# Performance work log

Measured on AMD Instinct MI355X. Metric: run time of the kernel, lower is better.

## Reference

```python
import jax, jax.numpy as jnp
import numpy as np

EPS = 1e-5  # torch LayerNorm default

def ln(x, g, b):
    mu = jnp.mean(x, axis=-1, keepdims=True)
    var = jnp.mean((x - mu) ** 2, axis=-1, keepdims=True)
    return (x - mu) * jax.lax.rsqrt(var + EPS) * g + b

B, S, E, A = 131072, 199, 3, 32
D_IN = S + 1  # state_dim + 1 (time feature)

def setup_inputs() -> dict:
    key = jax.random.key(0)
    ks = iter(jax.random.split(key, 32))
    def w(shape, fan_in):
        lim = 1.0 / np.sqrt(fan_in)
        return jax.random.uniform(next(ks), shape, jnp.float32, -lim, lim)
    inp = {
        "state": jax.random.normal(next(ks), (B, S), jnp.float32),
        "time_delta": jax.random.uniform(next(ks), (B,), jnp.float32),
        # trunk: Linear(200,256)+LN, Linear(256,256)+LN, Linear(256,128)+LN
        "W1": w((D_IN, 256), D_IN), "b1": w((256,), D_IN),
        "g1": jnp.ones((256,), jnp.float32), "be1": jnp.zeros((256,), jnp.float32),
        "W2": w((256, 256), 256), "b2": w((256,), 256),
        "g2": jnp.ones((256,), jnp.float32), "be2": jnp.zeros((256,), jnp.float32),
        "W3": w((256, 128), 256), "b3": w((128,), 256),
        "g3": jnp.ones((128,), jnp.float32), "be3": jnp.zeros((128,), jnp.float32),
        # value stream
        "Wv1": w((128, 64), 128), "bv1": w((64,), 128),
        "gv": jnp.ones((64,), jnp.float32), "bev": jnp.zeros((64,), jnp.float32),
        "Wv2": w((64, 1), 64), "bv2": w((1,), 64),
        # E stacked advantage streams (all heads share action dim A)
        "Wa1": w((E, 128, 64), 128), "ba1": w((E, 64), 128),
        "ga": jnp.ones((E, 64), jnp.float32), "bea": jnp.zeros((E, 64), jnp.float32),
        "Wa2": w((E, 64, A), 64), "ba2": w((E, A), 64),
        "event_type": jax.random.randint(next(ks), (B,), 0, E),
    }
    return inp

def reference(state, time_delta,
              W1, b1, g1, be1, W2, b2, g2, be2, W3, b3, g3, be3,
              Wv1, bv1, gv, bev, Wv2, bv2,
              Wa1, ba1, ga, bea, Wa2, ba2, event_type):
    td = time_delta[:, None]                       # [B,1]
    x = jnp.concatenate([state, td], axis=1)       # [B,200]
    h = jax.nn.relu(ln(x @ W1 + b1, g1, be1))      # [B,256]
    h = jax.nn.relu(ln(h @ W2 + b2, g2, be2))      # [B,256]
    f = jax.nn.relu(ln(h @ W3 + b3, g3, be3))      # [B,128]
    v = jax.nn.relu(ln(f @ Wv1 + bv1, gv, bev)) @ Wv2 + bv2  # [B,1]
    # compute all E advantage heads, then per-sample select by event_type
    h1 = jnp.einsum('bd,edh->ebh', f, Wa1) + ba1[:, None, :]           # [E,B,64]
    h1 = jax.nn.relu(ln(h1, ga[:, None, :], bea[:, None, :]))
    adv_all = jnp.einsum('ebh,eha->eba', h1, Wa2) + ba2[:, None, :]    # [E,B,A]
    adv = jnp.take_along_axis(adv_all, event_type[None, :, None], axis=0)[0]  # [B,A]
    return v + (adv - adv.mean(axis=1, keepdims=True))
```

## Files before the change

### kernel.cpp

```cpp
#include <hip/hip_runtime.h>
#include <hip/hip_bf16.h>
#include <stdint.h>

#define DEV __device__ __forceinline__

typedef __attribute__((ext_vector_type(8))) short short8;
typedef __attribute__((ext_vector_type(4))) float floatx4;

constexpr int TM  = 64;
constexpr int NB  = 131072;
constexpr int AST = 264;

constexpr int OFF_W1 = 0;
constexpr int OFF_W2 = 57344;
constexpr int OFF_W3 = 122880;
constexpr int OFF_WH = 155648;
constexpr int OFF_WA2= 188416;
constexpr int NWQ    = 194560;

constexpr int C_B1=0, C_G1=256, C_BE1=512, C_B2=768, C_G2=1024, C_BE2=1280,
  C_B3=1536, C_G3=1664, C_BE3=1792, C_BV1=1920, C_GV=1984, C_BEV=2048,
  C_WV2=2112, C_BV2=2176, C_BA1=2180, C_GA=2372, C_BEA=2564, C_BA2=2756;
constexpr int NCONST=2852;

struct Ptrs {
  const float *state,*td,*W1,*b1,*g1,*be1,*W2,*b2,*g2,*be2,*W3,*b3,*g3,*be3,
    *Wv1,*bv1,*gv,*bev,*Wv2,*bv2,*Wa1,*ba1,*ga,*bea,*Wa2,*ba2;
  const int *et;
};

DEV unsigned short f2bf(float x){
  uint32_t u = __float_as_uint(x);
  u += 0x7fffu + ((u>>16)&1u);
  return (unsigned short)(u>>16);
}
DEV uint32_t f2bf_pk(float a, float b){
  float2 f2; f2.x=a; f2.y=b;
  __hip_bfloat162 h = __float22bfloat162_rn(f2);
  union { __hip_bfloat162 h; uint32_t u; } cv; cv.h = h;
  return cv.u;
}

__global__ void prep_kernel(Ptrs p, unsigned short* __restrict__ wq, float* __restrict__ cq){
  int idx = blockIdx.x*256 + threadIdx.x;
  if (idx < NWQ) {
    float v = 0.f;
    if (idx < OFF_W2) {
      int e = idx, w = e/14336, r = e%14336;
      int kc = r>>11, ct=(r>>9)&3, l=(r>>3)&63, j=r&7;
      int n = w*64 + ct*16 + (l&15);
      int k = kc*32 + (l>>4)*8 + j;
      if (k < 200) v = p.W1[k*256 + n];
      else if (k == 200) v = p.b1[n];
    } else if (idx < OFF_W3) {
      int e = idx-OFF_W2, w=e>>14, r=e&16383;
      int kc=r>>11, ct=(r>>9)&3, l=(r>>3)&63, j=r&7;
      int n = w*64 + ct*16 + (l&15);
      int k = kc*32 + (l>>4)*8 + j;
      v = p.W2[k*256 + n];
    } else if (idx < OFF_WH) {
      int e = idx-OFF_W3, w=e>>13, r=e&8191;
      int kc=r>>10, ct=(r>>9)&1, l=(r>>3)&63, j=r&7;
      int n = w*32 + ct*16 + (l&15);
      int k = kc*32 + (l>>4)*8 + j;
      v = p.W3[k*128 + n];
    } else if (idx < OFF_WA2) {
      int e = idx-OFF_WH, h=e>>13, r=e&8191;
      int kc=r>>11, ct=(r>>9)&3, l=(r>>3)&63, j=r&7;
      int n = ct*16 + (l&15);
      int k = kc*32 + (l>>4)*8 + j;
      v = (h<3) ? p.Wa1[h*8192 + k*64 + n] : p.Wv1[k*64 + n];
    } else {
      int e = idx-OFF_WA2, h=e>>11, r=e&2047;
      int kc=r>>10, ct=(r>>9)&1, l=(r>>3)&63, j=r&7;
      int n = ct*16 + (l&15);
      int k = kc*32 + (l>>4)*8 + j;
      v = p.Wa2[h*2048 + k*32 + n];
    }
    wq[idx] = f2bf(v);
  } else if (idx < NWQ + NCONST) {
    int ci = idx - NWQ;
    float v;
    if      (ci < 256)  v = p.b1[ci];
    else if (ci < 512)  v = p.g1[ci-256];
    else if (ci < 768)  v = p.be1[ci-512];
    else if (ci < 1024) v = p.b2[ci-768];
    else if (ci < 1280) v = p.g2[ci-1024];
    else if (ci < 1536) v = p.be2[ci-1280];
    else if (ci < 1664) v = p.b3[ci-1536];
    else if (ci < 1792) v = p.g3[ci-1664];
    else if (ci < 1920) v = p.be3[ci-1792];
    else if (ci < 1984) v = p.bv1[ci-1920];
    else if (ci < 2048) v = p.gv[ci-1984];
    else if (ci < 2112) v = p.bev[ci-2048];
    else if (ci < 2176) v = p.Wv2[ci-2112];
    else if (ci < 2180) v = (ci==2176) ? p.bv2[0] : 0.f;
    else if (ci < 2372) v = p.ba1[ci-2180];
    else if (ci < 2564) v = p.ga[ci-2372];
    else if (ci < 2756) v = p.bea[ci-2564];
    else                v = p.ba2[ci-2756];
    cq[ci] = v;
  }
}

template<int N>
DEV void loadB(short8 (&B)[N], const unsigned short* __restrict__ src, int lane){
  #pragma unroll
  for (int i=0;i<N;i++) B[i] = *(const short8*)(src + i*512 + lane*8);
}

template<int RT>
DEV void zeroAccT(floatx4 (&acc)[RT][4]){
  const floatx4 z = {0.f,0.f,0.f,0.f};
  #pragma unroll
  for (int rt=0;rt<RT;rt++)
    #pragma unroll
    for (int ct=0;ct<4;ct++) acc[rt][ct]=z;
}

template<int KC,int RT>
DEV void runGemmT(floatx4 (&acc)[RT][4], const short8 (&Bw)[KC*RT],
                  const unsigned short* aBase, int aOff){
  #pragma unroll
  for (int kc=0;kc<KC;kc++){
    short8 a[4];
    #pragma unroll
    for (int ct=0;ct<4;ct++)
      a[ct] = *(const short8*)(aBase + ct*16*AST + aOff + kc*32);
    #pragma unroll
    for (int rt=0;rt<RT;rt++)
      #pragma unroll
      for (int ct=0;ct<4;ct++)
        acc[rt][ct] = __builtin_amdgcn_mfma_f32_16x16x32_bf16(Bw[kc*RT+rt], a[ct], acc[rt][ct], 0,0,0);
  }
}

template<int RT,bool BIAS>
DEV void statsT(floatx4 (&acc)[RT][4], const float* __restrict__ cq, int bo,
                float* sbuf, float* ssbuf, int q, int ln){
  if constexpr (BIAS){
    #pragma unroll
    for (int rt=0;rt<RT;rt++){
      floatx4 b4 = *(const floatx4*)(cq + bo + rt*16 + q*4);
      #pragma unroll
      for (int ct=0;ct<4;ct++) acc[rt][ct] += b4;
    }
  }
  #pragma unroll
  for (int ct=0;ct<4;ct++){
    float s=0.f, ss=0.f;
    #pragma unroll
    for (int rt=0;rt<RT;rt++)
      #pragma unroll
      for (int r=0;r<4;r++){ float v=acc[rt][ct][r]; s+=v; ss+=v*v; }
    s += __shfl_xor(s,16); ss += __shfl_xor(ss,16);
    s += __shfl_xor(s,32); ss += __shfl_xor(ss,32);
    if (q==0){
      atomicAdd(&sbuf[ct*16+ln], s);
      atomicAdd(&ssbuf[ct*16+ln], ss);
    }
  }
}

template<int RT>
DEV void lnWriteT(const floatx4 (&acc)[RT][4], const float* __restrict__ cq, int go, int beo,
                  const float* sbuf, const float* ssbuf, float invN,
                  unsigned short* act_, int colBase, int q, int ln){
  float mu[4], rs[4];
  #pragma unroll
  for (int ct=0;ct<4;ct++){
    float sv = sbuf[ct*16+ln], ssv = ssbuf[ct*16+ln];
    mu[ct] = sv*invN;
    rs[ct] = rsqrtf(ssv*invN - mu[ct]*mu[ct] + 1e-5f);
  }
  #pragma unroll
  for (int rt=0;rt<RT;rt++){
    floatx4 g4  = *(const floatx4*)(cq + go  + rt*16 + q*4);
    floatx4 be4 = *(const floatx4*)(cq + beo + rt*16 + q*4);
    #pragma unroll
    for (int ct=0;ct<4;ct++){
      float y[4];
      #pragma unroll
      for (int r=0;r<4;r++)
        y[r] = fmaxf((acc[rt][ct][r]-mu[ct])*rs[ct]*g4[r]+be4[r], 0.f);
      uint2 pk; pk.x = f2bf_pk(y[0],y[1]); pk.y = f2bf_pk(y[2],y[3]);
      *(uint2*)(act_ + (ct*16+ln)*AST + colBase + rt*16 + q*4) = pk;
    }
  }
}

__global__ __launch_bounds__(256,4) void dqn_main(
    const float* __restrict__ state, const float* __restrict__ td,
    const int* __restrict__ et, const unsigned short* __restrict__ wq,
    const float* __restrict__ cq, float* __restrict__ out)
{
  __shared__ __align__(16) unsigned short act[TM*AST];
  __shared__ float sstat[2][2][64];
  __shared__ float vbuf[64];
  __shared__ int   etl[64];

  const int tid=threadIdx.x, w=tid>>6, lane=tid&63, q=lane>>4, ln=lane&15;
  const int rowBlk = blockIdx.x*TM;

  {
    ((float*)sstat)[tid] = 0.f;
    const float* sbase = state + (size_t)rowBlk*199;
    #pragma unroll
    for (int it=0; it<7; ++it){
      int t = tid + it*256;
      int r = t/28, c = t - r*28;
      unsigned short* dst = act + r*AST + c*8;
      if (c < 25){
        const float* src = sbase + r*199 + c*8;
        float v0=src[0], v1=src[1], v2=src[2], v3=src[3];
        float v4=src[4], v5=src[5], v6=src[6];
        int o7 = (c==24)? 198 : c*8+7;
        float s7 = sbase[r*199 + o7];
        float v7 = (c==24)? td[rowBlk+r] : s7;
        uint4 pk;
        pk.x=f2bf_pk(v0,v1); pk.y=f2bf_pk(v2,v3);
        pk.z=f2bf_pk(v4,v5); pk.w=f2bf_pk(v6,v7);
        *(uint4*)dst = pk;
      } else {
        uint4 pk{0u,0u,0u,0u};
        if (c==25) pk.x = 0x3F80u;
        *(uint4*)dst = pk;
      }
    }
    if (tid < 64) etl[tid] = et[rowBlk+tid];
  }
  __syncthreads();

  const unsigned short* aBase = act + ln*AST + q*8;
  floatx4 acc[4][4];

  {
    short8 Bw[28];
    loadB<28>(Bw, wq + OFF_W1 + w*14336, lane);
    zeroAccT<4>(acc);
    runGemmT<7,4>(acc, Bw, aBase, 0);
  }
  statsT<4,false>(acc, cq, 0, sstat[0][0], sstat[0][1], q, ln);
  __syncthreads();
  lnWriteT<4>(acc, cq, C_G1+w*64, C_BE1+w*64, sstat[0][0], sstat[0][1], 1.f/256.f, act, w*64, q, ln);
  __syncthreads();

  {
    short8 Bw[32];
    loadB<32>(Bw, wq + OFF_W2 + w*16384, lane);
    zeroAccT<4>(acc);
    runGemmT<8,4>(acc, Bw, aBase, 0);
  }
  statsT<4,true>(acc, cq, C_B2+w*64, sstat[1][0], sstat[1][1], q, ln);
  __syncthreads();
  if (tid < 128) ((float*)sstat[0])[tid] = 0.f;
  lnWriteT<4>(acc, cq, C_G2+w*64, C_BE2+w*64, sstat[1][0], sstat[1][1], 1.f/256.f, act, w*64, q, ln);
  __syncthreads();

  floatx4 acc3[2][4];
  {
    short8 Bw[16];
    loadB<16>(Bw, wq + OFF_W3 + w*8192, lane);
    zeroAccT<2>(acc3);
    runGemmT<8,2>(acc3, Bw, aBase, 0);
  }
  statsT<2,true>(acc3, cq, C_B3+w*32, sstat[0][0], sstat[0][1], q, ln);
  __syncthreads();
  lnWriteT<2>(acc3, cq, C_G3+w*32, C_BE3+w*32, sstat[0][0], sstat[0][1], 1.f/128.f, act, w*32, q, ln);
  __syncthreads();

  {
    short8 Bh[16];
    loadB<16>(Bh, wq + OFF_WH + w*8192, lane);
    zeroAccT<4>(acc);
    runGemmT<4,4>(acc, Bh, aBase, 0);
  }
  {
    const int bo = (w<3)? C_BA1+w*64 : C_BV1;
    const int go = (w<3)? C_GA +w*64 : C_GV;
    const int beo= (w<3)? C_BEA+w*64 : C_BEV;
    #pragma unroll
    for (int rt=0;rt<4;rt++){
      floatx4 b4 = *(const floatx4*)(cq + bo + rt*16 + q*4);
      #pragma unroll
      for (int ct=0;ct<4;ct++) acc[rt][ct] += b4;
    }
    float mu[4], rs[4];
    #pragma unroll
    for (int ct=0;ct<4;ct++){
      float s=0.f, ss=0.f;
      #pragma unroll
      for (int rt=0;rt<4;rt++)
        #pragma unroll
        for (int r=0;r<4;r++){ float v=acc[rt][ct][r]; s+=v; ss+=v*v; }
      s += __shfl_xor(s,16); ss += __shfl_xor(ss,16);
      s += __shfl_xor(s,32); ss += __shfl_xor(ss,32);
      mu[ct]=s*(1.f/64.f);
      rs[ct]=rsqrtf(ss*(1.f/64.f)-mu[ct]*mu[ct]+1e-5f);
    }
    #pragma unroll
    for (int rt=0;rt<4;rt++){
      floatx4 g4  = *(const floatx4*)(cq + go  + rt*16 + q*4);
      floatx4 be4 = *(const floatx4*)(cq + beo + rt*16 + q*4);
      #pragma unroll
      for (int ct=0;ct<4;ct++)
        #pragma unroll
        for (int r=0;r<4;r++)
          acc[rt][ct][r] = fmaxf((acc[rt][ct][r]-mu[ct])*rs[ct]*g4[r]+be4[r], 0.f);
    }
    if (w==3){
      float bv2v = cq[C_BV2];
      floatx4 wv4[4];
      #pragma unroll
      for (int rt=0;rt<4;rt++) wv4[rt] = *(const floatx4*)(cq + C_WV2 + rt*16 + q*4);
      #pragma unroll
      for (int ct=0;ct<4;ct++){
        float dot=0.f;
        #pragma unroll
        for (int rt=0;rt<4;rt++)
          #pragma unroll
          for (int r=0;r<4;r++) dot += acc[rt][ct][r]*wv4[rt][r];
        dot += __shfl_xor(dot,16);
        dot += __shfl_xor(dot,32);
        if (q==0) vbuf[ct*16+ln] = dot + bv2v;
      }
    }
  }
  __syncthreads();

  if (w<3){
    #pragma unroll
    for (int rt=0;rt<4;rt++)
      #pragma unroll
      for (int ct=0;ct<4;ct++){
        uint2 pk;
        pk.x = f2bf_pk(acc[rt][ct][0], acc[rt][ct][1]);
        pk.y = f2bf_pk(acc[rt][ct][2], acc[rt][ct][3]);
        *(uint2*)(act + (ct*16+ln)*AST + 64*w + rt*16 + q*4) = pk;
      }
    short8 B2[4];
    loadB<4>(B2, wq + OFF_WA2 + w*2048, lane);
    floatx4 acc2[2][4];
    zeroAccT<2>(acc2);
    runGemmT<2,2>(acc2, B2, aBase, 64*w);
    #pragma unroll
    for (int rt=0;rt<2;rt++){
      floatx4 b4 = *(const floatx4*)(cq + C_BA2 + w*32 + rt*16 + q*4);
      #pragma unroll
      for (int ct=0;ct<4;ct++) acc2[rt][ct] += b4;
    }
    #pragma unroll
    for (int ct=0;ct<4;ct++){
      float sm=0.f;
      #pragma unroll
      for (int rt=0;rt<2;rt++)
        #pragma unroll
        for (int r=0;r<4;r++) sm += acc2[rt][ct][r];
      sm += __shfl_xor(sm,16);
      sm += __shfl_xor(sm,32);
      int b = ct*16+ln;
      if (etl[b]==w){
        float vm = vbuf[b] - sm*(1.f/32.f);
        #pragma unroll
        for (int rt=0;rt<2;rt++){
          floatx4 o = acc2[rt][ct];
          o[0]+=vm; o[1]+=vm; o[2]+=vm; o[3]+=vm;
          *(floatx4*)(out + (size_t)(rowBlk+b)*32 + rt*16 + q*4) = o;
        }
      }
    }
  }
}

extern "C" void kernel_launch(void* const* d_in, const int* in_sizes, int n_in,
                              void* d_out, int out_size, void* d_ws, size_t ws_size,
                              hipStream_t stream)
{
  Ptrs p;
  p.state=(const float*)d_in[0];  p.td =(const float*)d_in[1];
  p.W1 =(const float*)d_in[2];  p.b1 =(const float*)d_in[3];  p.g1 =(const float*)d_in[4];  p.be1=(const float*)d_in[5];
  p.W2 =(const float*)d_in[6];  p.b2 =(const float*)d_in[7];  p.g2 =(const float*)d_in[8];  p.be2=(const float*)d_in[9];
  p.W3 =(const float*)d_in[10]; p.b3 =(const float*)d_in[11]; p.g3 =(const float*)d_in[12]; p.be3=(const float*)d_in[13];
  p.Wv1=(const float*)d_in[14]; p.bv1=(const float*)d_in[15]; p.gv =(const float*)d_in[16]; p.bev=(const float*)d_in[17];
  p.Wv2=(const float*)d_in[18]; p.bv2=(const float*)d_in[19];
  p.Wa1=(const float*)d_in[20]; p.ba1=(const float*)d_in[21]; p.ga =(const float*)d_in[22]; p.bea=(const float*)d_in[23];
  p.Wa2=(const float*)d_in[24]; p.ba2=(const float*)d_in[25];
  p.et =(const int*)d_in[26];

  unsigned short* wq = (unsigned short*)d_ws;
  float* cq = (float*)((char*)d_ws + (size_t)NWQ*2);

  const int prepN = NWQ + NCONST;
  hipLaunchKernelGGL(prep_kernel, dim3((prepN+255)/256), dim3(256), 0, stream, p, wq, cq);
  hipLaunchKernelGGL(dqn_main, dim3(NB/TM), dim3(256), 0, stream,
                     p.state, p.td, p.et, (const unsigned short*)wq, (const float*)cq, (float*)d_out);
}
```

Measured before the change: 284.8 us.

## Split work across eight waves per block and stream weights inside GEMM loop

Doubles the block to 512 threads (8 waves), so each wave owns half as many output columns in the trunk layers. In the head stage, wave pairs split the 64 rows. Weights are no longer preloaded into large register arrays; each weight fragment is loaded from global memory just before the MFMAs that use it. This cuts register pressure and aims to raise latency hiding through more waves, at the cost of exposing global weight loads inside the inner loop and of redundant A-fragment loads from LDS across waves.

```diff
diff --git a/kernel.cpp b/kernel.cpp
--- a/kernel.cpp
+++ b/kernel.cpp
@@ -103,35 +103,31 @@
   }
 }
 
-template<int N>
-DEV void loadB(short8 (&B)[N], const unsigned short* __restrict__ src, int lane){
-  #pragma unroll
-  for (int i=0;i<N;i++) B[i] = *(const short8*)(src + i*512 + lane*8);
-}
-
-template<int RT>
-DEV void zeroAccT(floatx4 (&acc)[RT][4]){
+template<int RT,int CT>
+DEV void zeroAccT(floatx4 (&acc)[RT][CT]){
   const floatx4 z = {0.f,0.f,0.f,0.f};
   #pragma unroll
   for (int rt=0;rt<RT;rt++)
     #pragma unroll
-    for (int ct=0;ct<4;ct++) acc[rt][ct]=z;
-}
-
-template<int KC,int RT>
-DEV void runGemmT(floatx4 (&acc)[RT][4], const short8 (&Bw)[KC*RT],
-                  const unsigned short* aBase, int aOff){
+    for (int ct=0;ct<CT;ct++) acc[rt][ct]=z;
+}
+
+template<int KC,int RT,int CT>
+DEV void runGemmTW(floatx4 (&acc)[RT][CT], const unsigned short* __restrict__ wp, int kcStride,
+                   const unsigned short* aB, int aOff, int lane){
   #pragma unroll
   for (int kc=0;kc<KC;kc++){
-    short8 a[4];
-    #pragma unroll
-    for (int ct=0;ct<4;ct++)
-      a[ct] = *(const short8*)(aBase + ct*16*AST + aOff + kc*32);
-    #pragma unroll
-    for (int rt=0;rt<RT;rt++)
-      #pragma unroll
-      for (int ct=0;ct<4;ct++)
-        acc[rt][ct] = __builtin_amdgcn_mfma_f32_16x16x32_bf16(Bw[kc*RT+rt], a[ct], acc[rt][ct], 0,0,0);
+    short8 a[CT];
+    #pragma unroll
+    for (int c=0;c<CT;c++)
+      a[c] = *(const short8*)(aB + c*16*AST + aOff + kc*32);
+    #pragma unroll
+    for (int rt=0;rt<RT;rt++){
+      short8 bw = *(const short8*)(wp + kc*kcStride + rt*512 + lane*8);
+      #pragma unroll
+      for (int c=0;c<CT;c++)
+        acc[rt][c] = __builtin_amdgcn_mfma_f32_16x16x32_bf16(bw, a[c], acc[rt][c], 0,0,0);
+    }
   }
 }
 
@@ -189,7 +185,7 @@
   }
 }
 
-__global__ __launch_bounds__(256,4) void dqn_main(
+__global__ __launch_bounds__(512,6) void dqn_main(
     const float* __restrict__ state, const float* __restrict__ td,
     const int* __restrict__ et, const unsigned short* __restrict__ wq,
     const float* __restrict__ cq, float* __restrict__ out)
@@ -203,28 +199,30 @@
   const int rowBlk = blockIdx.x*TM;
 
   {
-    ((float*)sstat)[tid] = 0.f;
+    if (tid < 256) ((float*)sstat)[tid] = 0.f;
     const float* sbase = state + (size_t)rowBlk*199;
     #pragma unroll
-    for (int it=0; it<7; ++it){
-      int t = tid + it*256;
-      int r = t/28, c = t - r*28;
-      unsigned short* dst = act + r*AST + c*8;
-      if (c < 25){
-        const float* src = sbase + r*199 + c*8;
-        float v0=src[0], v1=src[1], v2=src[2], v3=src[3];
-        float v4=src[4], v5=src[5], v6=src[6];
-        int o7 = (c==24)? 198 : c*8+7;
-        float s7 = sbase[r*199 + o7];
-        float v7 = (c==24)? td[rowBlk+r] : s7;
-        uint4 pk;
-        pk.x=f2bf_pk(v0,v1); pk.y=f2bf_pk(v2,v3);
-        pk.z=f2bf_pk(v4,v5); pk.w=f2bf_pk(v6,v7);
-        *(uint4*)dst = pk;
-      } else {
-        uint4 pk{0u,0u,0u,0u};
-        if (c==25) pk.x = 0x3F80u;
-        *(uint4*)dst = pk;
+    for (int it=0; it<4; ++it){
+      int t = tid + it*512;
+      if (t < 1792){
+        int r = t/28, c = t - r*28;
+        unsigned short* dst = act + r*AST + c*8;
+        if (c < 25){
+          const float* src = sbase + r*199 + c*8;
+          float v0=src[0], v1=src[1], v2=src[2], v3=src[3];
+          float v4=src[4], v5=src[5], v6=src[6];
+          int o7 = (c==24)? 198 : c*8+7;
+          float s7 = sbase[r*199 + o7];
+          float v7 = (c==24)? td[rowBlk+r] : s7;
+          uint4 pk;
+          pk.x=f2bf_pk(v0,v1); pk.y=f2bf_pk(v2,v3);
+          pk.z=f2bf_pk(v4,v5); pk.w=f2bf_pk(v6,v7);
+          *(uint4*)dst = pk;
+        } else {
+          uint4 pk{0u,0u,0u,0u};
+          if (c==25) pk.x = 0x3F80u;
+          *(uint4*)dst = pk;
+        }
       }
     }
     if (tid < 64) etl[tid] = et[rowBlk+tid];
@@ -232,67 +230,66 @@
   __syncthreads();
 
   const unsigned short* aBase = act + ln*AST + q*8;
-  floatx4 acc[4][4];
-
-  {
-    short8 Bw[28];
-    loadB<28>(Bw, wq + OFF_W1 + w*14336, lane);
-    zeroAccT<4>(acc);
-    runGemmT<7,4>(acc, Bw, aBase, 0);
-  }
-  statsT<4,false>(acc, cq, 0, sstat[0][0], sstat[0][1], q, ln);
-  __syncthreads();
-  lnWriteT<4>(acc, cq, C_G1+w*64, C_BE1+w*64, sstat[0][0], sstat[0][1], 1.f/256.f, act, w*64, q, ln);
-  __syncthreads();
-
-  {
-    short8 Bw[32];
-    loadB<32>(Bw, wq + OFF_W2 + w*16384, lane);
-    zeroAccT<4>(acc);
-    runGemmT<8,4>(acc, Bw, aBase, 0);
-  }
-  statsT<4,true>(acc, cq, C_B2+w*64, sstat[1][0], sstat[1][1], q, ln);
+  floatx4 acc[2][4];
+
+  {
+    const unsigned short* wp = wq + OFF_W1 + (w>>1)*14336 + (w&1)*1024;
+    zeroAccT<2,4>(acc);
+    runGemmTW<7,2,4>(acc, wp, 2048, aBase, 0, lane);
+  }
+  statsT<2,false>(acc, cq, 0, sstat[0][0], sstat[0][1], q, ln);
+  __syncthreads();
+  lnWriteT<2>(acc, cq, C_G1+w*32, C_BE1+w*32, sstat[0][0], sstat[0][1], 1.f/256.f, act, w*32, q, ln);
+  __syncthreads();
+
+  {
+    const unsigned short* wp = wq + OFF_W2 + (w>>1)*16384 + (w&1)*1024;
+    zeroAccT<2,4>(acc);
+    runGemmTW<8,2,4>(acc, wp, 2048, aBase, 0, lane);
+  }
+  statsT<2,true>(acc, cq, C_B2+w*32, sstat[1][0], sstat[1][1], q, ln);
   __syncthreads();
   if (tid < 128) ((float*)sstat[0])[tid] = 0.f;
-  lnWriteT<4>(acc, cq, C_G2+w*64, C_BE2+w*64, sstat[1][0], sstat[1][1], 1.f/256.f, act, w*64, q, ln);
-  __syncthreads();
-
-  floatx4 acc3[2][4];
-  {
-    short8 Bw[16];
-    loadB<16>(Bw, wq + OFF_W3 + w*8192, lane);
-    zeroAccT<2>(acc3);
-    runGemmT<8,2>(acc3, Bw, aBase, 0);
-  }
-  statsT<2,true>(acc3, cq, C_B3+w*32, sstat[0][0], sstat[0][1], q, ln);
-  __syncthreads();
-  lnWriteT<2>(acc3, cq, C_G3+w*32, C_BE3+w*32, sstat[0][0], sstat[0][1], 1.f/128.f, act, w*32, q, ln);
-  __syncthreads();
-
-  {
-    short8 Bh[16];
-    loadB<16>(Bh, wq + OFF_WH + w*8192, lane);
-    zeroAccT<4>(acc);
-    runGemmT<4,4>(acc, Bh, aBase, 0);
-  }
-  {
-    const int bo = (w<3)? C_BA1+w*64 : C_BV1;
-    const int go = (w<3)? C_GA +w*64 : C_GV;
-    const int beo= (w<3)? C_BEA+w*64 : C_BEV;
+  lnWriteT<2>(acc, cq, C_G2+w*32, C_BE2+w*32, sstat[1][0], sstat[1][1], 1.f/256.f, act, w*32, q, ln);
+  __syncthreads();
+
+  floatx4 acc3[1][4];
+  {
+    const unsigned short* wp = wq + OFF_W3 + (w>>1)*8192 + (w&1)*512;
+    zeroAccT<1,4>(acc3);
+    runGemmTW<8,1,4>(acc3, wp, 1024, aBase, 0, lane);
+  }
+  statsT<1,true>(acc3, cq, C_B3+w*16, sstat[0][0], sstat[0][1], q, ln);
+  __syncthreads();
+  lnWriteT<1>(acc3, cq, C_G3+w*16, C_BE3+w*16, sstat[0][0], sstat[0][1], 1.f/128.f, act, w*16, q, ln);
+  __syncthreads();
+
+  const int h = w>>1, bh = w&1;
+  const unsigned short* aBaseH = act + (bh*32 + ln)*AST + q*8;
+  floatx4 acch[4][2];
+  {
+    const unsigned short* wp = wq + OFF_WH + h*8192;
+    zeroAccT<4,2>(acch);
+    runGemmTW<4,4,2>(acch, wp, 2048, aBaseH, 0, lane);
+  }
+  {
+    const int bo = (h<3)? C_BA1+h*64 : C_BV1;
+    const int go = (h<3)? C_GA +h*64 : C_GV;
+    const int beo= (h<3)? C_BEA+h*64 : C_BEV;
     #pragma unroll
     for (int rt=0;rt<4;rt++){
       floatx4 b4 = *(const floatx4*)(cq + bo + rt*16 + q*4);
       #pragma unroll
-      for (int ct=0;ct<4;ct++) acc[rt][ct] += b4;
-    }
-    float mu[4], rs[4];
-    #pragma unroll
-    for (int ct=0;ct<4;ct++){
+      for (int ct=0;ct<2;ct++) acch[rt][ct] += b4;
+    }
+    float mu[2], rs[2];
+    #pragma unroll
+    for (int ct=0;ct<2;ct++){
       float s=0.f, ss=0.f;
       #pragma unroll
       for (int rt=0;rt<4;rt++)
         #pragma unroll
-        for (int r=0;r<4;r++){ float v=acc[rt][ct][r]; s+=v; ss+=v*v; }
+        for (int r=0;r<4;r++){ float v=acch[rt][ct][r]; s+=v; ss+=v*v; }
       s += __shfl_xor(s,16); ss += __shfl_xor(ss,16);
       s += __shfl_xor(s,32); ss += __shfl_xor(ss,32);
       mu[ct]=s*(1.f/64.f);
@@ -303,54 +300,55 @@
       floatx4 g4  = *(const floatx4*)(cq + go  + rt*16 + q*4);
       floatx4 be4 = *(const floatx4*)(cq + beo + rt*16 + q*4);
       #pragma unroll
-      for (int ct=0;ct<4;ct++)
+      for (int ct=0;ct<2;ct++)
         #pragma unroll
         for (int r=0;r<4;r++)
-          acc[rt][ct][r] = fmaxf((acc[rt][ct][r]-mu[ct])*rs[ct]*g4[r]+be4[r], 0.f);
-    }
-    if (w==3){
+          acch[rt][ct][r] = fmaxf((acch[rt][ct][r]-mu[ct])*rs[ct]*g4[r]+be4[r], 0.f);
+    }
+    if (h==3){
       float bv2v = cq[C_BV2];
       floatx4 wv4[4];
       #pragma unroll
       for (int rt=0;rt<4;rt++) wv4[rt] = *(const floatx4*)(cq + C_WV2 + rt*16 + q*4);
       #pragma unroll
-      for (int ct=0;ct<4;ct++){
+      for (int ct=0;ct<2;ct++){
         float dot=0.f;
         #pragma unroll
         for (int rt=0;rt<4;rt++)
           #pragma unroll
-          for (int r=0;r<4;r++) dot += acc[rt][ct][r]*wv4[rt][r];
+          for (int r=0;r<4;r++) dot += acch[rt][ct][r]*wv4[rt][r];
         dot += __shfl_xor(dot,16);
         dot += __shfl_xor(dot,32);
-        if (q==0) vbuf[ct*16+ln] = dot + bv2v;
+        if (q==0) vbuf[(bh*2+ct)*16+ln] = dot + bv2v;
       }
     }
   }
   __syncthreads();
 
-  if (w<3){
+  if (h<3){
     #pragma unroll
     for (int rt=0;rt<4;rt++)
       #pragma unroll
-      for (int ct=0;ct<4;ct++){
+      for (int ct=0;ct<2;ct++){
         uint2 pk;
-        pk.x = f2bf_pk(acc[rt][ct][0], acc[rt][ct][1]);
-        pk.y = f2bf_pk(acc[rt][ct][2], acc[rt][ct][3]);
-        *(uint2*)(act + (ct*16+ln)*AST + 64*w + rt*16 + q*4) = pk;
+        pk.x = f2bf_pk(acch[rt][ct][0], acch[rt][ct][1]);
+        pk.y = f2bf_pk(acch[rt][ct][2], acch[rt][ct][3]);
+        *(uint2*)(act + ((bh*2+ct)*16+ln)*AST + 64*h + rt*16 + q*4) = pk;
       }
-    short8 B2[4];
-    loadB<4>(B2, wq + OFF_WA2 + w*2048, lane);
-    floatx4 acc2[2][4];
-    zeroAccT<2>(acc2);
-    runGemmT<2,2>(acc2, B2, aBase, 64*w);
+    floatx4 acc2[2][2];
+    {
+      const unsigned short* wp = wq + OFF_WA2 + h*2048;
+      zeroAccT<2,2>(acc2);
+      runGemmTW<2,2,2>(acc2, wp, 1024, aBaseH, 64*h, lane);
+    }
     #pragma unroll
     for (int rt=0;rt<2;rt++){
-      floatx4 b4 = *(const floatx4*)(cq + C_BA2 + w*32 + rt*16 + q*4);
-      #pragma unroll
-      for (int ct=0;ct<4;ct++) acc2[rt][ct] += b4;
-    }
-    #pragma unroll
-    for (int ct=0;ct<4;ct++){
+      floatx4 b4 = *(const floatx4*)(cq + C_BA2 + h*32 + rt*16 + q*4);
+      #pragma unroll
+      for (int ct=0;ct<2;ct++) acc2[rt][ct] += b4;
+    }
+    #pragma unroll
+    for (int ct=0;ct<2;ct++){
       float sm=0.f;
       #pragma unroll
       for (int rt=0;rt<2;rt++)
@@ -358,8 +356,8 @@
         for (int r=0;r<4;r++) sm += acc2[rt][ct][r];
       sm += __shfl_xor(sm,16);
       sm += __shfl_xor(sm,32);
-      int b = ct*16+ln;
-      if (etl[b]==w){
+      int b = (bh*2+ct)*16+ln;
+      if (etl[b]==h){
         float vm = vbuf[b] - sm*(1.f/32.f);
         #pragma unroll
         for (int rt=0;rt<2;rt++){
@@ -392,6 +390,6 @@
 
   const int prepN = NWQ + NCONST;
   hipLaunchKernelGGL(prep_kernel, dim3((prepN+255)/256), dim3(256), 0, stream, p, wq, cq);
-  hipLaunchKernelGGL(dqn_main, dim3(NB/TM), dim3(256), 0, stream,
+  hipLaunchKernelGGL(dqn_main, dim3(NB/TM), dim3(512), 0, stream,
                      p.state, p.td, p.et, (const unsigned short*)wq, (const float*)cq, (float*)d_out);
 }
```

Result: no change. 287.0 us (+0.8%).

## Interleave two 64-row tiles per block and read layer-1 input straight from global

Applied to the files above, without the earlier changes.

Each block now handles 128 rows as two 64-row tiles, each with its own LDS activation buffer. The stages are staggered so one tile's GEMM runs between the other tile's stats barrier and its LayerNorm write, halving barrier stalls per tile. Layer 1 builds its bf16 operand fragments directly from global fp32 state instead of staging them in LDS first. Weights are loaded from global inside each k-step rather than preloaded into register arrays. Occupancy drops from 4 to 2 blocks per CU and there are half as many blocks, while the uncoalesced strided global reads in layer 1 add memory traffic.

```diff
diff --git a/kernel.cpp b/kernel.cpp
--- a/kernel.cpp
+++ b/kernel.cpp
@@ -10,6 +10,8 @@
 constexpr int TM  = 64;
 constexpr int NB  = 131072;
 constexpr int AST = 264;
+
+struct F4 { float x,y,z,w; };
 
 constexpr int OFF_W1 = 0;
 constexpr int OFF_W2 = 57344;
@@ -34,7 +36,7 @@
   u += 0x7fffu + ((u>>16)&1u);
   return (unsigned short)(u>>16);
 }
-DEV uint32_t f2bf_pk(float a, float b){
+DEV uint32_t pkbf(float a, float b){
   float2 f2; f2.x=a; f2.y=b;
   __hip_bfloat162 h = __float22bfloat162_rn(f2);
   union { __hip_bfloat162 h; uint32_t u; } cv; cv.h = h;
@@ -103,12 +105,6 @@
   }
 }
 
-template<int N>
-DEV void loadB(short8 (&B)[N], const unsigned short* __restrict__ src, int lane){
-  #pragma unroll
-  for (int i=0;i<N;i++) B[i] = *(const short8*)(src + i*512 + lane*8);
-}
-
 template<int RT>
 DEV void zeroAccT(floatx4 (&acc)[RT][4]){
   const floatx4 z = {0.f,0.f,0.f,0.f};
@@ -119,19 +115,59 @@
 }
 
 template<int KC,int RT>
-DEV void runGemmT(floatx4 (&acc)[RT][4], const short8 (&Bw)[KC*RT],
-                  const unsigned short* aBase, int aOff){
+DEV void runGemmW(floatx4 (&acc)[RT][4], const unsigned short* __restrict__ wp,
+                  const unsigned short* __restrict__ aB, int aOff, int lane){
   #pragma unroll
   for (int kc=0;kc<KC;kc++){
     short8 a[4];
     #pragma unroll
-    for (int ct=0;ct<4;ct++)
-      a[ct] = *(const short8*)(aBase + ct*16*AST + aOff + kc*32);
-    #pragma unroll
-    for (int rt=0;rt<RT;rt++)
-      #pragma unroll
-      for (int ct=0;ct<4;ct++)
-        acc[rt][ct] = __builtin_amdgcn_mfma_f32_16x16x32_bf16(Bw[kc*RT+rt], a[ct], acc[rt][ct], 0,0,0);
+    for (int c=0;c<4;c++)
+      a[c] = *(const short8*)(aB + c*16*AST + aOff + kc*32);
+    #pragma unroll
+    for (int rt=0;rt<RT;rt++){
+      short8 bw = *(const short8*)(wp + (kc*RT+rt)*512 + lane*8);
+      #pragma unroll
+      for (int c=0;c<4;c++)
+        acc[rt][c] = __builtin_amdgcn_mfma_f32_16x16x32_bf16(bw, a[c], acc[rt][c], 0,0,0);
+    }
+  }
+}
+
+DEV void gemmL1G(floatx4 (&acc)[4][4], const unsigned short* __restrict__ wp,
+                 const float* __restrict__ xb, const float* __restrict__ tdp,
+                 int lane){
+  const int q=lane>>4, ln=lane&15;
+  #pragma unroll
+  for (int kc=0;kc<7;kc++){
+    short8 bfr[4];
+    #pragma unroll
+    for (int ct=0;ct<4;ct++){
+      const float* rp = xb + (size_t)(ct*16+ln)*199;
+      uint32_t w0,w1,w2,w3;
+      if (kc<6){
+        F4 lo = *(const F4*)(rp + kc*32 + q*8);
+        F4 hi = *(const F4*)(rp + kc*32 + q*8 + 4);
+        w0=pkbf(lo.x,lo.y); w1=pkbf(lo.z,lo.w); w2=pkbf(hi.x,hi.y); w3=pkbf(hi.z,hi.w);
+      } else if (q==0){
+        F4 lo = *(const F4*)(rp + 192);
+        float v4=rp[196], v5=rp[197], v6=rp[198], v7=tdp[ct*16+ln];
+        w0=pkbf(lo.x,lo.y); w1=pkbf(lo.z,lo.w); w2=pkbf(v4,v5); w3=pkbf(v6,v7);
+      } else if (q==1){
+        w0=0x3F80u; w1=0u; w2=0u; w3=0u;
+      } else {
+        w0=0u; w1=0u; w2=0u; w3=0u;
+      }
+      union { uint32_t u[4]; short8 s; } cv;
+      cv.u[0]=w0; cv.u[1]=w1; cv.u[2]=w2; cv.u[3]=w3;
+      bfr[ct]=cv.s;
+    }
+    #pragma unroll
+    for (int rt=0;rt<4;rt++){
+      short8 bw = *(const short8*)(wp + (kc*4+rt)*512 + lane*8);
+      #pragma unroll
+      for (int c=0;c<4;c++)
+        acc[rt][c] = __builtin_amdgcn_mfma_f32_16x16x32_bf16(bw, bfr[c], acc[rt][c], 0,0,0);
+    }
   }
 }
 
@@ -183,193 +219,183 @@
       #pragma unroll
       for (int r=0;r<4;r++)
         y[r] = fmaxf((acc[rt][ct][r]-mu[ct])*rs[ct]*g4[r]+be4[r], 0.f);
-      uint2 pk; pk.x = f2bf_pk(y[0],y[1]); pk.y = f2bf_pk(y[2],y[3]);
+      uint2 pk; pk.x = pkbf(y[0],y[1]); pk.y = pkbf(y[2],y[3]);
       *(uint2*)(act_ + (ct*16+ln)*AST + colBase + rt*16 + q*4) = pk;
     }
   }
 }
 
-__global__ __launch_bounds__(256,4) void dqn_main(
+DEV void headPhase(floatx4 (&acc)[4][4], const float* __restrict__ cq,
+                   const unsigned short* __restrict__ wq,
+                   const unsigned short* __restrict__ actb, float* vb,
+                   int w, int lane, int q, int ln){
+  zeroAccT<4>(acc);
+  runGemmW<4,4>(acc, wq + OFF_WH + w*8192, actb + ln*AST + q*8, 0, lane);
+  const int bo = (w<3)? C_BA1+w*64 : C_BV1;
+  const int go = (w<3)? C_GA +w*64 : C_GV;
+  const int beo= (w<3)? C_BEA+w*64 : C_BEV;
+  #pragma unroll
+  for (int rt=0;rt<4;rt++){
+    floatx4 b4 = *(const floatx4*)(cq + bo + rt*16 + q*4);
+    #pragma unroll
+    for (int ct=0;ct<4;ct++) acc[rt][ct] += b4;
+  }
+  float mu[4], rs[4];
+  #pragma unroll
+  for (int ct=0;ct<4;ct++){
+    float s=0.f, ss=0.f;
+    #pragma unroll
+    for (int rt=0;rt<4;rt++)
+      #pragma unroll
+      for (int r=0;r<4;r++){ float v=acc[rt][ct][r]; s+=v; ss+=v*v; }
+    s += __shfl_xor(s,16); ss += __shfl_xor(ss,16);
+    s += __shfl_xor(s,32); ss += __shfl_xor(ss,32);
+    mu[ct]=s*(1.f/64.f);
+    rs[ct]=rsqrtf(ss*(1.f/64.f)-mu[ct]*mu[ct]+1e-5f);
+  }
+  #pragma unroll
+  for (int rt=0;rt<4;rt++){
+    floatx4 g4  = *(const floatx4*)(cq + go  + rt*16 + q*4);
+    floatx4 be4 = *(const floatx4*)(cq + beo + rt*16 + q*4);
+    #pragma unroll
+    for (int ct=0;ct<4;ct++)
+      #pragma unroll
+      for (int r=0;r<4;r++)
+        acc[rt][ct][r] = fmaxf((acc[rt][ct][r]-mu[ct])*rs[ct]*g4[r]+be4[r], 0.f);
+  }
+  if (w==3){
+    float bv2v = cq[C_BV2];
+    floatx4 wv4[4];
+    #pragma unroll
+    for (int rt=0;rt<4;rt++) wv4[rt] = *(const floatx4*)(cq + C_WV2 + rt*16 + q*4);
+    #pragma unroll
+    for (int ct=0;ct<4;ct++){
+      float dot=0.f;
+      #pragma unroll
+      for (int rt=0;rt<4;rt++)
+        #pragma unroll
+        for (int r=0;r<4;r++) dot += acc[rt][ct][r]*wv4[rt][r];
+      dot += __shfl_xor(dot,16);
+      dot += __shfl_xor(dot,32);
+      if (q==0) vb[ct*16+ln] = dot + bv2v;
+    }
+  }
+}
+
+DEV void advPhase(const floatx4 (&acc)[4][4], const float* __restrict__ cq,
+                  const unsigned short* __restrict__ wq,
+                  unsigned short* actb, const float* vb, const int* etlT,
+                  float* __restrict__ outT, int w, int lane, int q, int ln){
+  #pragma unroll
+  for (int rt=0;rt<4;rt++)
+    #pragma unroll
+    for (int ct=0;ct<4;ct++){
+      uint2 pk;
+      pk.x = pkbf(acc[rt][ct][0], acc[rt][ct][1]);
+      pk.y = pkbf(acc[rt][ct][2], acc[rt][ct][3]);
+      *(uint2*)(actb + (ct*16+ln)*AST + 64*w + rt*16 + q*4) = pk;
+    }
+  floatx4 acc2[2][4];
+  zeroAccT<2>(acc2);
+  runGemmW<2,2>(acc2, wq + OFF_WA2 + w*2048, actb + ln*AST + q*8, 64*w, lane);
+  #pragma unroll
+  for (int rt=0;rt<2;rt++){
+    floatx4 b4 = *(const floatx4*)(cq + C_BA2 + w*32 + rt*16 + q*4);
+    #pragma unroll
+    for (int ct=0;ct<4;ct++) acc2[rt][ct] += b4;
+  }
+  #pragma unroll
+  for (int ct=0;ct<4;ct++){
+    float sm=0.f;
+    #pragma unroll
+    for (int rt=0;rt<2;rt++)
+      #pragma unroll
+      for (int r=0;r<4;r++) sm += acc2[rt][ct][r];
+    sm += __shfl_xor(sm,16);
+    sm += __shfl_xor(sm,32);
+    int b = ct*16+ln;
+    if (etlT[b]==w){
+      float vm = vb[b] - sm*(1.f/32.f);
+      #pragma unroll
+      for (int rt=0;rt<2;rt++){
+        floatx4 o = acc2[rt][ct];
+        o[0]+=vm; o[1]+=vm; o[2]+=vm; o[3]+=vm;
+        *(floatx4*)(outT + (size_t)b*32 + rt*16 + q*4) = o;
+      }
+    }
+  }
+}
+
+__global__ __launch_bounds__(256,2) void dqn_main(
     const float* __restrict__ state, const float* __restrict__ td,
     const int* __restrict__ et, const unsigned short* __restrict__ wq,
     const float* __restrict__ cq, float* __restrict__ out)
 {
-  __shared__ __align__(16) unsigned short act[TM*AST];
-  __shared__ float sstat[2][2][64];
-  __shared__ float vbuf[64];
-  __shared__ int   etl[64];
+  __shared__ __align__(16) unsigned short actA[TM*AST];
+  __shared__ __align__(16) unsigned short actB[TM*AST];
+  __shared__ float sstat[2][3][2][64];
+  __shared__ float vbuf[2][64];
+  __shared__ int   etl[2][64];
 
   const int tid=threadIdx.x, w=tid>>6, lane=tid&63, q=lane>>4, ln=lane&15;
-  const int rowBlk = blockIdx.x*TM;
-
-  {
-    ((float*)sstat)[tid] = 0.f;
-    const float* sbase = state + (size_t)rowBlk*199;
-    #pragma unroll
-    for (int it=0; it<7; ++it){
-      int t = tid + it*256;
-      int r = t/28, c = t - r*28;
-      unsigned short* dst = act + r*AST + c*8;
-      if (c < 25){
-        const float* src = sbase + r*199 + c*8;
-        float v0=src[0], v1=src[1], v2=src[2], v3=src[3];
-        float v4=src[4], v5=src[5], v6=src[6];
-        int o7 = (c==24)? 198 : c*8+7;
-        float s7 = sbase[r*199 + o7];
-        float v7 = (c==24)? td[rowBlk+r] : s7;
-        uint4 pk;
-        pk.x=f2bf_pk(v0,v1); pk.y=f2bf_pk(v2,v3);
-        pk.z=f2bf_pk(v4,v5); pk.w=f2bf_pk(v6,v7);
-        *(uint4*)dst = pk;
-      } else {
-        uint4 pk{0u,0u,0u,0u};
-        if (c==25) pk.x = 0x3F80u;
-        *(uint4*)dst = pk;
-      }
-    }
-    if (tid < 64) etl[tid] = et[rowBlk+tid];
-  }
-  __syncthreads();
-
-  const unsigned short* aBase = act + ln*AST + q*8;
-  floatx4 acc[4][4];
-
-  {
-    short8 Bw[28];
-    loadB<28>(Bw, wq + OFF_W1 + w*14336, lane);
-    zeroAccT<4>(acc);
-    runGemmT<7,4>(acc, Bw, aBase, 0);
-  }
-  statsT<4,false>(acc, cq, 0, sstat[0][0], sstat[0][1], q, ln);
-  __syncthreads();
-  lnWriteT<4>(acc, cq, C_G1+w*64, C_BE1+w*64, sstat[0][0], sstat[0][1], 1.f/256.f, act, w*64, q, ln);
-  __syncthreads();
-
-  {
-    short8 Bw[32];
-    loadB<32>(Bw, wq + OFF_W2 + w*16384, lane);
-    zeroAccT<4>(acc);
-    runGemmT<8,4>(acc, Bw, aBase, 0);
-  }
-  statsT<4,true>(acc, cq, C_B2+w*64, sstat[1][0], sstat[1][1], q, ln);
-  __syncthreads();
-  if (tid < 128) ((float*)sstat[0])[tid] = 0.f;
-  lnWriteT<4>(acc, cq, C_G2+w*64, C_BE2+w*64, sstat[1][0], sstat[1][1], 1.f/256.f, act, w*64, q, ln);
-  __syncthreads();
-
-  floatx4 acc3[2][4];
-  {
-    short8 Bw[16];
-    loadB<16>(Bw, wq + OFF_W3 + w*8192, lane);
-    zeroAccT<2>(acc3);
-    runGemmT<8,2>(acc3, Bw, aBase, 0);
-  }
-  statsT<2,true>(acc3, cq, C_B3+w*32, sstat[0][0], sstat[0][1], q, ln);
-  __syncthreads();
-  lnWriteT<2>(acc3, cq, C_G3+w*32, C_BE3+w*32, sstat[0][0], sstat[0][1], 1.f/128.f, act, w*32, q, ln);
-  __syncthreads();
-
-  {
-    short8 Bh[16];
-    loadB<16>(Bh, wq + OFF_WH + w*8192, lane);
-    zeroAccT<4>(acc);
-    runGemmT<4,4>(acc, Bh, aBase, 0);
-  }
-  {
-    const int bo = (w<3)? C_BA1+w*64 : C_BV1;
-    const int go = (w<3)? C_GA +w*64 : C_GV;
-    const int beo= (w<3)? C_BEA+w*64 : C_BEV;
-    #pragma unroll
-    for (int rt=0;rt<4;rt++){
-      floatx4 b4 = *(const floatx4*)(cq + bo + rt*16 + q*4);
-      #pragma unroll
-      for (int ct=0;ct<4;ct++) acc[rt][ct] += b4;
-    }
-    float mu[4], rs[4];
-    #pragma unroll
-    for (int ct=0;ct<4;ct++){
-      float s=0.f, ss=0.f;
-      #pragma unroll
-      for (int rt=0;rt<4;rt++)
-        #pragma unroll
-        for (int r=0;r<4;r++){ float v=acc[rt][ct][r]; s+=v; ss+=v*v; }
-      s += __shfl_xor(s,16); ss += __shfl_xor(ss,16);
-      s += __shfl_xor(s,32); ss += __shfl_xor(ss,32);
-      mu[ct]=s*(1.f/64.f);
-      rs[ct]=rsqrtf(ss*(1.f/64.f)-mu[ct]*mu[ct]+1e-5f);
-    }
-    #pragma unroll
-    for (int rt=0;rt<4;rt++){
-      floatx4 g4  = *(const floatx4*)(cq + go  + rt*16 + q*4);
-      floatx4 be4 = *(const floatx4*)(cq + beo + rt*16 + q*4);
-      #pragma unroll
-      for (int ct=0;ct<4;ct++)
-        #pragma unroll
-        for (int r=0;r<4;r++)
-          acc[rt][ct][r] = fmaxf((acc[rt][ct][r]-mu[ct])*rs[ct]*g4[r]+be4[r], 0.f);
-    }
-    if (w==3){
-      float bv2v = cq[C_BV2];
-      floatx4 wv4[4];
-      #pragma unroll
-      for (int rt=0;rt<4;rt++) wv4[rt] = *(const floatx4*)(cq + C_WV2 + rt*16 + q*4);
-      #pragma unroll
-      for (int ct=0;ct<4;ct++){
-        float dot=0.f;
-        #pragma unroll
-        for (int rt=0;rt<4;rt++)
-          #pragma unroll
-          for (int r=0;r<4;r++) dot += acc[rt][ct][r]*wv4[rt][r];
-        dot += __shfl_xor(dot,16);
-        dot += __shfl_xor(dot,32);
-        if (q==0) vbuf[ct*16+ln] = dot + bv2v;
-      }
-    }
-  }
-  __syncthreads();
-
-  if (w<3){
-    #pragma unroll
-    for (int rt=0;rt<4;rt++)
-      #pragma unroll
-      for (int ct=0;ct<4;ct++){
-        uint2 pk;
-        pk.x = f2bf_pk(acc[rt][ct][0], acc[rt][ct][1]);
-        pk.y = f2bf_pk(acc[rt][ct][2], acc[rt][ct][3]);
-        *(uint2*)(act + (ct*16+ln)*AST + 64*w + rt*16 + q*4) = pk;
-      }
-    short8 B2[4];
-    loadB<4>(B2, wq + OFF_WA2 + w*2048, lane);
-    floatx4 acc2[2][4];
-    zeroAccT<2>(acc2);
-    runGemmT<2,2>(acc2, B2, aBase, 64*w);
-    #pragma unroll
-    for (int rt=0;rt<2;rt++){
-      floatx4 b4 = *(const floatx4*)(cq + C_BA2 + w*32 + rt*16 + q*4);
-      #pragma unroll
-      for (int ct=0;ct<4;ct++) acc2[rt][ct] += b4;
-    }
-    #pragma unroll
-    for (int ct=0;ct<4;ct++){
-      float sm=0.f;
-      #pragma unroll
-      for (int rt=0;rt<2;rt++)
-        #pragma unroll
-        for (int r=0;r<4;r++) sm += acc2[rt][ct][r];
-      sm += __shfl_xor(sm,16);
-      sm += __shfl_xor(sm,32);
-      int b = ct*16+ln;
-      if (etl[b]==w){
-        float vm = vbuf[b] - sm*(1.f/32.f);
-        #pragma unroll
-        for (int rt=0;rt<2;rt++){
-          floatx4 o = acc2[rt][ct];
-          o[0]+=vm; o[1]+=vm; o[2]+=vm; o[3]+=vm;
-          *(floatx4*)(out + (size_t)(rowBlk+b)*32 + rt*16 + q*4) = o;
-        }
-      }
-    }
-  }
+  const int rowBlk = blockIdx.x*128;
+  const float* x0 = state + (size_t)rowBlk*199;
+  const float* x1 = x0 + (size_t)64*199;
+
+  ((float*)sstat)[tid]     = 0.f;
+  ((float*)sstat)[tid+256] = 0.f;
+  ((float*)sstat)[tid+512] = 0.f;
+  if (tid < 128) ((int*)etl)[tid] = et[rowBlk+tid];
+  __syncthreads();
+
+  floatx4 aT0[4][4], aT1[4][4];
+
+  zeroAccT<4>(aT0);
+  gemmL1G(aT0, wq + OFF_W1 + w*14336, x0, td + rowBlk, lane);
+  statsT<4,false>(aT0, cq, 0, sstat[0][0][0], sstat[0][0][1], q, ln);
+  __syncthreads();
+
+  lnWriteT<4>(aT0, cq, C_G1+w*64, C_BE1+w*64, sstat[0][0][0], sstat[0][0][1], 1.f/256.f, actA, w*64, q, ln);
+  zeroAccT<4>(aT1);
+  gemmL1G(aT1, wq + OFF_W1 + w*14336, x1, td + rowBlk + 64, lane);
+  statsT<4,false>(aT1, cq, 0, sstat[1][0][0], sstat[1][0][1], q, ln);
+  __syncthreads();
+
+  lnWriteT<4>(aT1, cq, C_G1+w*64, C_BE1+w*64, sstat[1][0][0], sstat[1][0][1], 1.f/256.f, actB, w*64, q, ln);
+  zeroAccT<4>(aT0);
+  runGemmW<8,4>(aT0, wq + OFF_W2 + w*16384, actA + ln*AST + q*8, 0, lane);
+  statsT<4,true>(aT0, cq, C_B2+w*64, sstat[0][1][0], sstat[0][1][1], q, ln);
+  __syncthreads();
+
+  lnWriteT<4>(aT0, cq, C_G2+w*64, C_BE2+w*64, sstat[0][1][0], sstat[0][1][1], 1.f/256.f, actA, w*64, q, ln);
+  zeroAccT<4>(aT1);
+  runGemmW<8,4>(aT1, wq + OFF_W2 + w*16384, actB + ln*AST + q*8, 0, lane);
+  statsT<4,true>(aT1, cq, C_B2+w*64, sstat[1][1][0], sstat[1][1][1], q, ln);
+  __syncthreads();
+
+  lnWriteT<4>(aT1, cq, C_G2+w*64, C_BE2+w*64, sstat[1][1][0], sstat[1][1][1], 1.f/256.f, actB, w*64, q, ln);
+  floatx4 c3T0[2][4];
+  zeroAccT<2>(c3T0);
+  runGemmW<8,2>(c3T0, wq + OFF_W3 + w*8192, actA + ln*AST + q*8, 0, lane);
+  statsT<2,true>(c3T0, cq, C_B3+w*32, sstat[0][2][0], sstat[0][2][1], q, ln);
+  __syncthreads();
+
+  lnWriteT<2>(c3T0, cq, C_G3+w*32, C_BE3+w*32, sstat[0][2][0], sstat[0][2][1], 1.f/128.f, actA, w*32, q, ln);
+  floatx4 c3T1[2][4];
+  zeroAccT<2>(c3T1);
+  runGemmW<8,2>(c3T1, wq + OFF_W3 + w*8192, actB + ln*AST + q*8, 0, lane);
+  statsT<2,true>(c3T1, cq, C_B3+w*32, sstat[1][2][0], sstat[1][2][1], q, ln);
+  __syncthreads();
+
+  lnWriteT<2>(c3T1, cq, C_G3+w*32, C_BE3+w*32, sstat[1][2][0], sstat[1][2][1], 1.f/128.f, actB, w*32, q, ln);
+  headPhase(aT0, cq, wq, actA, vbuf[0], w, lane, q, ln);
+  __syncthreads();
+
+  headPhase(aT1, cq, wq, actB, vbuf[1], w, lane, q, ln);
+  if (w<3) advPhase(aT0, cq, wq, actA, vbuf[0], etl[0], out + (size_t)rowBlk*32, w, lane, q, ln);
+  __syncthreads();
+
+  if (w<3) advPhase(aT1, cq, wq, actB, vbuf[1], etl[1], out + (size_t)(rowBlk+64)*32, w, lane, q, ln);
 }
 
 extern "C" void kernel_launch(void* const* d_in, const int* in_sizes, int n_in,
@@ -392,6 +418,6 @@
 
   const int prepN = NWQ + NCONST;
   hipLaunchKernelGGL(prep_kernel, dim3((prepN+255)/256), dim3(256), 0, stream, p, wq, cq);
-  hipLaunchKernelGGL(dqn_main, dim3(NB/TM), dim3(256), 0, stream,
+  hipLaunchKernelGGL(dqn_main, dim3(NB/128), dim3(256), 0, stream,
                      p.state, p.td, p.et, (const unsigned short*)wq, (const float*)cq, (float*)d_out);
 }
```

Result: slower. 291.5 us (+2.3%).
